# Kernel optimization log

Hardware: AMD Instinct MI355X
Metric: run time of the kernel (lower is better)

Reference implementation:

```python
import jax, jax.numpy as jnp
import numpy as np

BIAS = 1.0
SIGMA = 0.5
EPS = 1e-5


def _mrf_loss(gen, tar):
    # gen, tar: [N, C, H, W]
    N, C, H, W = tar.shape
    meanT = jnp.mean(tar, axis=1, keepdims=True)
    g = gen - meanT
    t = tar - meanT
    g = g / jnp.linalg.norm(g, ord=2, axis=1, keepdims=True)
    t = t / jnp.linalg.norm(t, ord=2, axis=1, keepdims=True)
    # 1x1-patch conv2d with target patches as filters == per-pixel cosine
    # correlation matrix: [N, P=H*W (target positions), H, W (gen positions)]
    tp = t.reshape(N, C, H * W)
    cd = jnp.einsum('nchw,ncp->nphw', g, tp)
    cd = -(cd - 1.0) / 2.0  # cosine distance in [0, 1]
    div = jnp.min(cd, axis=1, keepdims=True)
    rel = cd / (div + EPS)
    e = jnp.exp((BIAS - rel) / SIGMA)
    cs = e / jnp.sum(e, axis=1, keepdims=True)  # sum-normalize over P
    k_max_nc = jnp.max(cs.reshape(N, H * W, -1), axis=2)  # max over gen HW
    div_mrf = jnp.mean(k_max_nc, axis=1)
    return jnp.sum(-jnp.log(div_mrf))


def setup_inputs() -> dict:
    key = jax.random.key(0)
    k1, k2, k3, k4 = jax.random.split(key, 4)
    return {
        'gen3': jax.random.normal(k1, (4, 256, 56, 56), dtype=jnp.float32),
        'tar3': jax.random.normal(k2, (4, 256, 56, 56), dtype=jnp.float32),
        'gen4': jax.random.normal(k3, (4, 512, 28, 28), dtype=jnp.float32),
        'tar4': jax.random.normal(k4, (4, 512, 28, 28), dtype=jnp.float32),
    }


def reference(gen3, tar3, gen4, tar4):
    # weights = [0, 0, 0.5, 1, 0] over VGG relu1..relu5 features
    return 0.5 * _mrf_loss(gen3, tar3) + 1.0 * _mrf_loss(gen4, tar4)
```

## Files before the change

### kernel.cpp

```cpp
#include <hip/hip_runtime.h>
#include <math.h>

typedef __bf16 bf16x8 __attribute__((ext_vector_type(8)));
typedef float f32x4 __attribute__((ext_vector_type(4)));

#define EPSV 1e-5f
#define GLB(p) ((__attribute__((address_space(1))) void*)(p))
#define LDS(p) ((__attribute__((address_space(3))) void*)(p))

__device__ __forceinline__ unsigned fkey(float f) {
  unsigned b = __float_as_uint(f);
  return (b & 0x80000000u) ? ~b : (b | 0x80000000u);
}
__device__ __forceinline__ float funkey(unsigned k) {
  return __uint_as_float((k & 0x80000000u) ? (k & 0x7fffffffu) : ~k);
}

__global__ __launch_bounds__(256) void norm_kernel(
    const float* __restrict__ g3, const float* __restrict__ t3,
    __bf16* __restrict__ G3, __bf16* __restrict__ T3,
    const float* __restrict__ g4, const float* __restrict__ t4,
    __bf16* __restrict__ G4, __bf16* __restrict__ T4)
{
  int lay = blockIdx.z >> 2, n = blockIdx.z & 3;
  const float *gen, *tar; __bf16 *Gh, *Th; int C, P, Ppad, PT, NWORK, NTOT, NG;
  if (lay == 0) { gen = g3; tar = t3; Gh = G3; Th = T3; C = 256; P = 3136; Ppad = 3200; PT = 32; NWORK = 98; NTOT = 100; NG = 8; }
  else          { gen = g4; tar = t4; Gh = G4; Th = T4; C = 512; P = 784;  Ppad = 896;  PT = 16; NWORK = 49; NTOT = 56;  NG = 16; }
  if (blockIdx.y >= (unsigned)NTOT) return;
  int pl, cg;
  if (lay == 0) { pl = threadIdx.x & 31; cg = threadIdx.x >> 5; }
  else          { pl = threadIdx.x & 15; cg = threadIdx.x >> 4; }
  int c0 = cg * 32;

  if (blockIdx.y >= (unsigned)NWORK) {
    int p = P + (blockIdx.y - NWORK) * PT + pl;
    if (p < Ppad) {
      __bf16* tp = Th + ((size_t)n * Ppad + p) * C + c0;
      __bf16* gp = Gh + ((size_t)n * Ppad + p) * C + c0;
      bf16x8 z;
      for (int j = 0; j < 8; j++) z[j] = (__bf16)0.f;
      for (int j = 0; j < 32; j += 8) { *(bf16x8*)(tp + j) = z; *(bf16x8*)(gp + j) = z; }
    }
    return;
  }

  int p = blockIdx.y * PT + pl;
  const float* tb = tar + (size_t)n * C * P + (size_t)c0 * P + p;
  const float* gb = gen + (size_t)n * C * P + (size_t)c0 * P + p;
  float tv[32], gv[32];
  float st = 0.f, sst = 0.f, sg = 0.f, ssg = 0.f;
#pragma unroll
  for (int j = 0; j < 32; j++) {
    tv[j] = tb[(size_t)j * P];
    gv[j] = gb[(size_t)j * P];
  }
#pragma unroll
  for (int j = 0; j < 32; j++) {
    st += tv[j]; sst += tv[j] * tv[j];
    sg += gv[j]; ssg += gv[j] * gv[j];
  }
  __shared__ f32x4 red[16][32];
  red[cg][pl] = f32x4{st, sst, sg, ssg};
  __syncthreads();
  for (int h = NG >> 1; h > 0; h >>= 1) {
    if (cg < h) {
      f32x4 a = red[cg][pl], b = red[cg + h][pl];
      red[cg][pl] = f32x4{a[0] + b[0], a[1] + b[1], a[2] + b[2], a[3] + b[3]};
    }
    __syncthreads();
  }
  f32x4 s = red[0][pl];
  float m = s[0] / (float)C;
  float vt = s[1] - s[0] * s[0] / (float)C;
  float vg = s[3] - 2.f * m * s[2] + (float)C * m * m;
  float it = rsqrtf(fmaxf(vt, 1e-30f));
  float ig = rsqrtf(fmaxf(vg, 1e-30f));
  __bf16* tp = Th + ((size_t)n * Ppad + p) * C + c0;
  __bf16* gp = Gh + ((size_t)n * Ppad + p) * C + c0;
#pragma unroll
  for (int j0 = 0; j0 < 32; j0 += 8) {
    bf16x8 to, go;
    for (int j = 0; j < 8; j++) {
      to[j] = (__bf16)((tv[j0 + j] - m) * it);
      go[j] = (__bf16)((gv[j0 + j] - m) * ig);
    }
    *(bf16x8*)(tp + j0) = to;
    *(bf16x8*)(gp + j0) = go;
  }
}

__global__ __launch_bounds__(256) void gemm_kernel(
    const __bf16* __restrict__ A3, const __bf16* __restrict__ B3,
    __bf16* __restrict__ So3, unsigned* __restrict__ dk3,
    const __bf16* __restrict__ A4, const __bf16* __restrict__ B4,
    __bf16* __restrict__ So4, unsigned* __restrict__ dk4)
{
  __shared__ __attribute__((aligned(16))) __bf16 As[4][4096];
  __shared__ __attribute__((aligned(16))) __bf16 Bs[4][4096];
  int lay = blockIdx.z >> 2, n = blockIdx.z & 3;
  const __bf16 *A, *B; __bf16* S; unsigned* dk; int C, Ppad, Qpad, Preal, NT;
  if (lay == 0) { A = A3; B = B3; S = So3; dk = dk3; C = 256; Ppad = 3200; Qpad = 3200; Preal = 3136; NT = 25; }
  else          { A = A4; B = B4; S = So4; dk = dk4; C = 512; Ppad = 896;  Qpad = 896;  Preal = 784;  NT = 7; }
  if (blockIdx.x >= (unsigned)NT || blockIdx.y >= (unsigned)NT) return;
  int p0 = blockIdx.y * 128, q0 = blockIdx.x * 128;
  int tid = threadIdx.x;
  int w = tid >> 6, lane = tid & 63;
  int lm = lane & 15, lq = lane >> 4;
  int wrow = (w >> 1) * 64, wcol = (w & 1) * 64;

  int srow = tid >> 2;
  int scol = (((tid & 3) ^ ((tid >> 3) & 3)) * 8);
  const __bf16* gA = A + ((size_t)n * Ppad + p0 + srow) * C + scol;
  const __bf16* gB = B + ((size_t)n * Qpad + q0 + srow) * C + scol;
  size_t rowoff = (size_t)64 * C;
  char* lAbase = (char*)&As[0][0] + w * 1024;
  char* lBbase = (char*)&Bs[0][0] + w * 1024;

  int sl = lq ^ ((lm >> 1) & 3);
  int aoff = (wrow + lm) * 64 + sl * 16;
  int boff = (wcol + lm) * 64 + sl * 16;

  f32x4 acc[4][4];
  for (int i = 0; i < 4; i++)
    for (int j = 0; j < 4; j++)
      acc[i][j] = f32x4{0.f, 0.f, 0.f, 0.f};

  auto issue = [&](int s) {
    int k0 = s << 5;
    char* a = lAbase + (s & 3) * 8192;
    char* b = lBbase + (s & 3) * 8192;
    __builtin_amdgcn_global_load_lds(GLB(gA + k0), LDS(a), 16, 0, 0);
    __builtin_amdgcn_global_load_lds(GLB(gA + rowoff + k0), LDS(a + 4096), 16, 0, 0);
    __builtin_amdgcn_global_load_lds(GLB(gB + k0), LDS(b), 16, 0, 0);
    __builtin_amdgcn_global_load_lds(GLB(gB + rowoff + k0), LDS(b + 4096), 16, 0, 0);
  };
  auto compute = [&](int it) {
    const char* ab = (const char*)&As[0][0] + (it & 3) * 8192;
    const char* bb = (const char*)&Bs[0][0] + (it & 3) * 8192;
    bf16x8 af[4], bf[4];
    for (int i = 0; i < 4; i++) af[i] = *(const bf16x8*)(ab + aoff + i * 1024);
    for (int j = 0; j < 4; j++) bf[j] = *(const bf16x8*)(bb + boff + j * 1024);
    for (int i = 0; i < 4; i++)
      for (int j = 0; j < 4; j++)
        acc[i][j] = __builtin_amdgcn_mfma_f32_16x16x32_bf16(af[i], bf[j], acc[i][j], 0, 0, 0);
  };

  int nk = C >> 5;
  issue(0); issue(1); issue(2);
  for (int it = 0; it < nk - 2; it++) {
    asm volatile("s_waitcnt vmcnt(8)" ::: "memory");
    __builtin_amdgcn_s_barrier();
    compute(it);
    if (it + 3 < nk) issue(it + 3);
  }
  asm volatile("s_waitcnt vmcnt(4)" ::: "memory");
  __builtin_amdgcn_s_barrier();
  compute(nk - 2);
  asm volatile("s_waitcnt vmcnt(0)" ::: "memory");
  __builtin_amdgcn_s_barrier();
  compute(nk - 1);

  __bf16* Sb = S + (size_t)n * Ppad * Qpad;
  float cm[4] = {-INFINITY, -INFINITY, -INFINITY, -INFINITY};
  for (int i = 0; i < 4; i++) {
    for (int j = 0; j < 4; j++) {
      for (int ri = 0; ri < 4; ri++) {
        int pr = p0 + wrow + i * 16 + lq * 4 + ri;
        int qc = q0 + wcol + j * 16 + lm;
        __bf16 bv = (__bf16)acc[i][j][ri];
        Sb[(size_t)pr * Qpad + qc] = bv;
        if (pr < Preal) cm[j] = fmaxf(cm[j], (float)bv);
      }
    }
  }
  for (int j = 0; j < 4; j++) {
    float v = cm[j];
    v = fmaxf(v, __shfl_xor(v, 16, 64));
    v = fmaxf(v, __shfl_xor(v, 32, 64));
    if (lq == 0 && v > -INFINITY) {
      int qc = q0 + wcol + j * 16 + lm;
      atomicMax(&dk[(size_t)n * Qpad + qc], fkey(v));
    }
  }
}

__global__ __launch_bounds__(256) void z_kernel(
    const __bf16* __restrict__ S3, const unsigned* __restrict__ dk3, float* __restrict__ Zp3,
    const __bf16* __restrict__ S4, const unsigned* __restrict__ dk4, float* __restrict__ Zp4)
{
  int lay = blockIdx.z >> 2, n = blockIdx.z & 3;
  const __bf16* S; const unsigned* dk; float* Zp;
  int Ppad, Qreal, Qpad, NSL, SLAB, NX;
  if (lay == 0) { S = S3; dk = dk3; Zp = Zp3; Ppad = 3200; Qreal = 3136; Qpad = 3200; NSL = 98; SLAB = 32; NX = 2; }
  else          { S = S4; dk = dk4; Zp = Zp4; Ppad = 896;  Qreal = 784;  Qpad = 896;  NSL = 49; SLAB = 16; NX = 1; }
  if (blockIdx.x >= (unsigned)NX || blockIdx.y >= (unsigned)NSL) return;
  int q = (blockIdx.x * 256 + threadIdx.x) * 8;
  if (q >= Qreal) return;
  float id[8], nid[8];
  const unsigned* dkp = dk + (size_t)n * Qpad + q;
#pragma unroll
  for (int j = 0; j < 8; j++) {
    float mx = funkey(dkp[j]);
    float d = 0.5f * (1.f - mx) + EPSV;
    id[j] = 1.f / d;
    nid[j] = -id[j];
  }
  int p0 = blockIdx.y * SLAB;
  const __bf16* Sp = S + (size_t)n * Ppad * Qpad + q;
  float acc[8] = {0.f, 0.f, 0.f, 0.f, 0.f, 0.f, 0.f, 0.f};
  for (int pb = 0; pb < SLAB; pb += 8) {
    bf16x8 sv[8];
#pragma unroll
    for (int r = 0; r < 8; r++)
      sv[r] = *(const bf16x8*)(Sp + (size_t)(p0 + pb + r) * Qpad);
#pragma unroll
    for (int r = 0; r < 8; r++)
      for (int j = 0; j < 8; j++)
        acc[j] += __expf(fmaf((float)sv[r][j], id[j], nid[j]));
  }
  float* zp = Zp + ((size_t)n * NSL + blockIdx.y) * Qpad + q;
  *(f32x4*)zp = f32x4{acc[0], acc[1], acc[2], acc[3]};
  *(f32x4*)(zp + 4) = f32x4{acc[4], acc[5], acc[6], acc[7]};
}

__global__ __launch_bounds__(256) void reduce_kernel(
    const float* __restrict__ Zp3, const unsigned* __restrict__ dk3,
    float* __restrict__ invd3, float* __restrict__ c3,
    const float* __restrict__ Zp4, const unsigned* __restrict__ dk4,
    float* __restrict__ invd4, float* __restrict__ c4)
{
  int lay = blockIdx.y >> 2, n = blockIdx.y & 3;
  const float* Zp; const unsigned* dk; float *invd, *c; int Qreal, Qpad, NSL;
  if (lay == 0) { Zp = Zp3; dk = dk3; invd = invd3; c = c3; Qreal = 3136; Qpad = 3200; NSL = 98; }
  else          { Zp = Zp4; dk = dk4; invd = invd4; c = c4; Qreal = 784;  Qpad = 896;  NSL = 49; }
  int q = blockIdx.x * 256 + threadIdx.x;
  if (q >= Qreal) return;
  float s0 = 0.f, s1 = 0.f, s2 = 0.f, s3 = 0.f;
  int sl = 0;
  for (; sl + 4 <= NSL; sl += 4) {
    s0 += Zp[((size_t)n * NSL + sl) * Qpad + q];
    s1 += Zp[((size_t)n * NSL + sl + 1) * Qpad + q];
    s2 += Zp[((size_t)n * NSL + sl + 2) * Qpad + q];
    s3 += Zp[((size_t)n * NSL + sl + 3) * Qpad + q];
  }
  for (; sl < NSL; sl++) s0 += Zp[((size_t)n * NSL + sl) * Qpad + q];
  float s = (s0 + s1) + (s2 + s3);
  float mx = funkey(dk[(size_t)n * Qpad + q]);
  float d = 0.5f * (1.f - mx) + EPSV;
  float idv = 1.f / d;
  invd[(size_t)n * Qpad + q] = idv;
  c[(size_t)n * Qpad + q] = -logf(s) - idv;
}

__global__ __launch_bounds__(256) void rowmax_kernel(
    const __bf16* __restrict__ S3, const float* __restrict__ invd3,
    const float* __restrict__ c3, float* __restrict__ km3,
    const __bf16* __restrict__ S4, const float* __restrict__ invd4,
    const float* __restrict__ c4, float* __restrict__ km4)
{
  int lay = blockIdx.y >> 2, n = blockIdx.y & 3;
  const __bf16* S; const float *invd, *cc; float* kmax;
  int Qreal, Qpad, Ppad, NB;
  if (lay == 0) { S = S3; invd = invd3; cc = c3; kmax = km3; Qreal = 3136; Qpad = 3200; Ppad = 3200; NB = 392; }
  else          { S = S4; invd = invd4; cc = c4; kmax = km4; Qreal = 784;  Qpad = 896;  Ppad = 896;  NB = 98; }
  if (blockIdx.x >= (unsigned)NB) return;
  int p0 = blockIdx.x * 8;
  const __bf16* Sp = S + ((size_t)n * Ppad + p0) * Qpad;
  const float* id = invd + (size_t)n * Qpad;
  const float* cp = cc + (size_t)n * Qpad;
  int nq8 = Qreal >> 3;
  float m[8];
#pragma unroll
  for (int r = 0; r < 8; r++) m[r] = -INFINITY;
  for (int i = threadIdx.x; i < nq8; i += 256) {
    f32x4 i0 = *(const f32x4*)(id + (size_t)i * 8);
    f32x4 i1 = *(const f32x4*)(id + (size_t)i * 8 + 4);
    f32x4 c0 = *(const f32x4*)(cp + (size_t)i * 8);
    f32x4 c1 = *(const f32x4*)(cp + (size_t)i * 8 + 4);
#pragma unroll
    for (int r = 0; r < 8; r++) {
      bf16x8 sv = *(const bf16x8*)(Sp + (size_t)r * Qpad + (size_t)i * 8);
      for (int j = 0; j < 4; j++)
        m[r] = fmaxf(m[r], fmaf((float)sv[j], i0[j], c0[j]));
      for (int j = 0; j < 4; j++)
        m[r] = fmaxf(m[r], fmaf((float)sv[j + 4], i1[j], c1[j]));
    }
  }
#pragma unroll
  for (int r = 0; r < 8; r++)
    for (int off = 32; off > 0; off >>= 1)
      m[r] = fmaxf(m[r], __shfl_xor(m[r], off, 64));
  __shared__ float red[4][8];
  int w = threadIdx.x >> 6;
  if ((threadIdx.x & 63) == 0)
    for (int r = 0; r < 8; r++) red[w][r] = m[r];
  __syncthreads();
  if (threadIdx.x < 8) {
    int r = threadIdx.x;
    float mr = fmaxf(fmaxf(red[0][r], red[1][r]), fmaxf(red[2][r], red[3][r]));
    kmax[(size_t)n * Ppad + p0 + r] = __expf(mr);
  }
}

__global__ void final_kernel(const float* __restrict__ kmax3, const float* __restrict__ kmax4,
                             float* __restrict__ out)
{
  __shared__ float red[256];
  int tid = threadIdx.x;
  float total = 0.f;
  for (int l = 0; l < 2; l++) {
    const float* km = l ? kmax4 : kmax3;
    int P = l ? 784 : 3136;
    int Ppad = l ? 896 : 3200;
    float wgt = l ? 1.0f : 0.5f;
    for (int n = 0; n < 4; n++) {
      float s = 0.f;
      for (int i = tid; i < P; i += 256) s += km[(size_t)n * Ppad + i];
      red[tid] = s;
      __syncthreads();
      for (int st = 128; st > 0; st >>= 1) {
        if (tid < st) red[tid] += red[tid + st];
        __syncthreads();
      }
      if (tid == 0) total += wgt * (-logf(red[0] / (float)P));
      __syncthreads();
    }
  }
  if (tid == 0) out[0] = total;
}

extern "C" void kernel_launch(void* const* d_in, const int* in_sizes, int n_in,
                              void* d_out, int out_size, void* d_ws, size_t ws_size,
                              hipStream_t stream)
{
  const float* gen3 = (const float*)d_in[0];
  const float* tar3 = (const float*)d_in[1];
  const float* gen4 = (const float*)d_in[2];
  const float* tar4 = (const float*)d_in[3];

  char* ws = (char*)d_ws;
  size_t off = 0;
  auto take = [&](size_t bytes) { char* p = ws + off; off += bytes; return p; };

  unsigned* divkey3 = (unsigned*)take(51200);
  unsigned* divkey4 = (unsigned*)take(14336);
  size_t zero_bytes = off;
  __bf16* That3 = (__bf16*)take(6553600);
  __bf16* Ghat3 = (__bf16*)take(6553600);
  __bf16* That4 = (__bf16*)take(3670016);
  __bf16* Ghat4 = (__bf16*)take(3670016);
  __bf16* S3    = (__bf16*)take(81920000);
  __bf16* S4    = (__bf16*)take(6422528);
  float*  Zp3   = (float*) take(5017600);
  float*  Zp4   = (float*) take(702464);
  float* invd3  = (float*)take(51200);
  float* c3     = (float*)take(51200);
  float* kmax3  = (float*)take(51200);
  float* invd4  = (float*)take(14336);
  float* c4     = (float*)take(14336);
  float* kmax4  = (float*)take(14336);

  hipMemsetAsync(divkey3, 0, zero_bytes, stream);

  norm_kernel<<<dim3(1, 100, 8), 256, 0, stream>>>(gen3, tar3, Ghat3, That3,
                                                   gen4, tar4, Ghat4, That4);
  gemm_kernel<<<dim3(25, 25, 8), 256, 0, stream>>>(That3, Ghat3, S3, divkey3,
                                                   That4, Ghat4, S4, divkey4);
  z_kernel<<<dim3(2, 98, 8), 256, 0, stream>>>(S3, divkey3, Zp3,
                                               S4, divkey4, Zp4);
  reduce_kernel<<<dim3(13, 8), 256, 0, stream>>>(Zp3, divkey3, invd3, c3,
                                                 Zp4, divkey4, invd4, c4);
  rowmax_kernel<<<dim3(392, 8), 256, 0, stream>>>(S3, invd3, c3, kmax3,
                                                  S4, invd4, c4, kmax4);
  final_kernel<<<1, 256, 0, stream>>>(kmax3, kmax4, (float*)d_out);
}
```

Measured before the change: 219.7 us.

## Compact GEMM grid with grouped tile order, LDS-staged vector stores, single-buffer loop

Replaces the padded 3D grid, where most layer-4 blocks exited immediately, with a flat 1D grid of only the live tiles. Tiles are assigned in groups of eight row-tiles for better L2 reuse of the operands. The output tile is staged through LDS so each thread writes 16-byte vectors to global memory instead of scattered 2-byte stores. The 4-stage async load pipeline is replaced by a single-buffered loop with two barriers per k-step, which cuts LDS use but exposes load latency unless other blocks hide it.

```diff
diff --git a/kernel.cpp b/kernel.cpp
--- a/kernel.cpp
+++ b/kernel.cpp
@@ -95,26 +95,38 @@
     const __bf16* __restrict__ A4, const __bf16* __restrict__ B4,
     __bf16* __restrict__ So4, unsigned* __restrict__ dk4)
 {
-  __shared__ __attribute__((aligned(16))) __bf16 As[4][4096];
-  __shared__ __attribute__((aligned(16))) __bf16 Bs[4][4096];
-  int lay = blockIdx.z >> 2, n = blockIdx.z & 3;
-  const __bf16 *A, *B; __bf16* S; unsigned* dk; int C, Ppad, Qpad, Preal, NT;
-  if (lay == 0) { A = A3; B = B3; S = So3; dk = dk3; C = 256; Ppad = 3200; Qpad = 3200; Preal = 3136; NT = 25; }
-  else          { A = A4; B = B4; S = So4; dk = dk4; C = 512; Ppad = 896;  Qpad = 896;  Preal = 784;  NT = 7; }
-  if (blockIdx.x >= (unsigned)NT || blockIdx.y >= (unsigned)NT) return;
-  int p0 = blockIdx.y * 128, q0 = blockIdx.x * 128;
+  __shared__ __attribute__((aligned(16))) char smem[36864];
+
+  int id = blockIdx.x;
+  const __bf16 *A, *B; __bf16* S; unsigned* dk;
+  int C, Ppad, Qpad, Preal, NT, n, t;
+  if (id < 2500) {
+    n = id / 625; t = id - n * 625;
+    A = A3; B = B3; S = So3; dk = dk3; C = 256; Ppad = 3200; Qpad = 3200; Preal = 3136; NT = 25;
+  } else {
+    id -= 2500;
+    n = id / 49; t = id - n * 49;
+    A = A4; B = B4; S = So4; dk = dk4; C = 512; Ppad = 896;  Qpad = 896;  Preal = 784;  NT = 7;
+  }
+  int bpb = NT * 8;
+  int b = t / bpb, r = t - b * bpb;
+  int rem = NT - b * 8;
+  int h = rem < 8 ? rem : 8;
+  int pt = b * 8 + r % h, qt = r / h;
+  int p0 = pt * 128, q0 = qt * 128;
+
   int tid = threadIdx.x;
   int w = tid >> 6, lane = tid & 63;
   int lm = lane & 15, lq = lane >> 4;
   int wrow = (w >> 1) * 64, wcol = (w & 1) * 64;
 
   int srow = tid >> 2;
-  int scol = (((tid & 3) ^ ((tid >> 3) & 3)) * 8);
+  int scol = ((tid & 3) ^ ((tid >> 3) & 3)) * 8;
   const __bf16* gA = A + ((size_t)n * Ppad + p0 + srow) * C + scol;
   const __bf16* gB = B + ((size_t)n * Qpad + q0 + srow) * C + scol;
   size_t rowoff = (size_t)64 * C;
-  char* lAbase = (char*)&As[0][0] + w * 1024;
-  char* lBbase = (char*)&Bs[0][0] + w * 1024;
+  char* lA = smem + w * 1024;
+  char* lB = smem + 16384 + w * 1024;
 
   int sl = lq ^ ((lm >> 1) & 3);
   int aoff = (wrow + lm) * 64 + sl * 16;
@@ -125,54 +137,47 @@
     for (int j = 0; j < 4; j++)
       acc[i][j] = f32x4{0.f, 0.f, 0.f, 0.f};
 
-  auto issue = [&](int s) {
-    int k0 = s << 5;
-    char* a = lAbase + (s & 3) * 8192;
-    char* b = lBbase + (s & 3) * 8192;
-    __builtin_amdgcn_global_load_lds(GLB(gA + k0), LDS(a), 16, 0, 0);
-    __builtin_amdgcn_global_load_lds(GLB(gA + rowoff + k0), LDS(a + 4096), 16, 0, 0);
-    __builtin_amdgcn_global_load_lds(GLB(gB + k0), LDS(b), 16, 0, 0);
-    __builtin_amdgcn_global_load_lds(GLB(gB + rowoff + k0), LDS(b + 4096), 16, 0, 0);
-  };
-  auto compute = [&](int it) {
-    const char* ab = (const char*)&As[0][0] + (it & 3) * 8192;
-    const char* bb = (const char*)&Bs[0][0] + (it & 3) * 8192;
+  for (int k0 = 0; k0 < C; k0 += 32) {
+    __syncthreads();
+    __builtin_amdgcn_global_load_lds(GLB(gA + k0), LDS(lA), 16, 0, 0);
+    __builtin_amdgcn_global_load_lds(GLB(gA + rowoff + k0), LDS(lA + 4096), 16, 0, 0);
+    __builtin_amdgcn_global_load_lds(GLB(gB + k0), LDS(lB), 16, 0, 0);
+    __builtin_amdgcn_global_load_lds(GLB(gB + rowoff + k0), LDS(lB + 4096), 16, 0, 0);
+    __syncthreads();
     bf16x8 af[4], bf[4];
-    for (int i = 0; i < 4; i++) af[i] = *(const bf16x8*)(ab + aoff + i * 1024);
-    for (int j = 0; j < 4; j++) bf[j] = *(const bf16x8*)(bb + boff + j * 1024);
+    for (int i = 0; i < 4; i++) af[i] = *(const bf16x8*)(smem + aoff + i * 1024);
+    for (int j = 0; j < 4; j++) bf[j] = *(const bf16x8*)(smem + 16384 + boff + j * 1024);
     for (int i = 0; i < 4; i++)
       for (int j = 0; j < 4; j++)
         acc[i][j] = __builtin_amdgcn_mfma_f32_16x16x32_bf16(af[i], bf[j], acc[i][j], 0, 0, 0);
-  };
-
-  int nk = C >> 5;
-  issue(0); issue(1); issue(2);
-  for (int it = 0; it < nk - 2; it++) {
-    asm volatile("s_waitcnt vmcnt(8)" ::: "memory");
-    __builtin_amdgcn_s_barrier();
-    compute(it);
-    if (it + 3 < nk) issue(it + 3);
-  }
-  asm volatile("s_waitcnt vmcnt(4)" ::: "memory");
-  __builtin_amdgcn_s_barrier();
-  compute(nk - 2);
-  asm volatile("s_waitcnt vmcnt(0)" ::: "memory");
-  __builtin_amdgcn_s_barrier();
-  compute(nk - 1);
-
-  __bf16* Sb = S + (size_t)n * Ppad * Qpad;
+  }
+
   float cm[4] = {-INFINITY, -INFINITY, -INFINITY, -INFINITY};
+  for (int i = 0; i < 4; i++)
+    for (int j = 0; j < 4; j++)
+      for (int ri = 0; ri < 4; ri++) {
+        int pr = p0 + wrow + i * 16 + lq * 4 + ri;
+        if (pr < Preal) cm[j] = fmaxf(cm[j], (float)(__bf16)acc[i][j][ri]);
+      }
+
+  __syncthreads();
   for (int i = 0; i < 4; i++) {
     for (int j = 0; j < 4; j++) {
-      for (int ri = 0; ri < 4; ri++) {
-        int pr = p0 + wrow + i * 16 + lq * 4 + ri;
-        int qc = q0 + wcol + j * 16 + lm;
-        __bf16 bv = (__bf16)acc[i][j][ri];
-        Sb[(size_t)pr * Qpad + qc] = bv;
-        if (pr < Preal) cm[j] = fmaxf(cm[j], (float)bv);
-      }
-    }
-  }
+      int row = wrow + i * 16 + lq * 4;
+      int col = wcol + j * 16 + lm;
+      for (int ri = 0; ri < 4; ri++)
+        *(__bf16*)(smem + (row + ri) * 288 + col * 2) = (__bf16)acc[i][j][ri];
+    }
+  }
+  __syncthreads();
+  __bf16* Sb = S + (size_t)n * Ppad * Qpad;
+  int rr = tid >> 4, cc8 = (tid & 15) * 8;
+  for (int r8 = 0; r8 < 8; r8++) {
+    int row = r8 * 16 + rr;
+    bf16x8 v = *(const bf16x8*)(smem + row * 288 + cc8 * 2);
+    *(bf16x8*)(Sb + (size_t)(p0 + row) * Qpad + q0 + cc8) = v;
+  }
+
   for (int j = 0; j < 4; j++) {
     float v = cm[j];
     v = fmaxf(v, __shfl_xor(v, 16, 64));
@@ -364,8 +369,8 @@
 
   norm_kernel<<<dim3(1, 100, 8), 256, 0, stream>>>(gen3, tar3, Ghat3, That3,
                                                    gen4, tar4, Ghat4, That4);
-  gemm_kernel<<<dim3(25, 25, 8), 256, 0, stream>>>(That3, Ghat3, S3, divkey3,
-                                                   That4, Ghat4, S4, divkey4);
+  gemm_kernel<<<2696, 256, 0, stream>>>(That3, Ghat3, S3, divkey3,
+                                        That4, Ghat4, S4, divkey4);
   z_kernel<<<dim3(2, 98, 8), 256, 0, stream>>>(S3, divkey3, Zp3,
                                                S4, divkey4, Zp4);
   reduce_kernel<<<dim3(13, 8), 256, 0, stream>>>(Zp3, divkey3, invd3, c3,
```

After: 205.3 us. 6.5% less time.
